# Kernel optimization log

Hardware: AMD Instinct MI355X
Metric: run time of the kernel (lower is better)

## Reference

```python
import jax, jax.numpy as jnp
import numpy as np

B, S, D, H = 64, 256, 2048, 16
HD = D // H

def setup_inputs() -> dict:
    key = jax.random.key(0)
    k1, k2, k3 = jax.random.split(key, 3)
    x = jax.random.normal(k1, (B, S, D), dtype=jnp.float32)
    # torch Linear weights: [out_features, in_features], scaled like kaiming-ish init
    w_qkv = jax.random.normal(k2, (3 * D, D), dtype=jnp.float32) * (1.0 / np.sqrt(D))
    w_o = jax.random.normal(k3, (D, D), dtype=jnp.float32) * (1.0 / np.sqrt(D))
    return {"x": x, "w_qkv": w_qkv, "w_o": w_o}

def reference(x, w_qkv, w_o):
    b, s, d = x.shape
    qkv = jnp.einsum('bsd,ed->bse', x, w_qkv)            # [B,S,3D]
    qkv = qkv.reshape(b, s, 3, H, HD).transpose(2, 0, 3, 1, 4)  # [3,B,H,S,HD]
    q, k, v = qkv[0], qkv[1], qkv[2]
    scores = jnp.einsum('bhqd,bhkd->bhqk', q, k) * (HD ** -0.5)  # [B,H,S,S]
    causal = jnp.triu(jnp.ones((s, s), dtype=bool), 1)
    scores = jnp.where(causal, jnp.float32(-1e9), scores)
    a = jax.nn.softmax(scores, axis=-1)
    ctx = jnp.einsum('bhqk,bhkd->bhqd', a, v)            # [B,H,S,HD]
    ctx = ctx.transpose(0, 2, 1, 3).reshape(b, s, d)     # [B,S,D]
    return jnp.einsum('bsd,ed->bse', ctx, w_o)
```

## Files before the change

### kernel.cpp

```cpp
#include <hip/hip_runtime.h>

#define NB 64
#define NS 256
#define ND 2048
#define NH 16
#define NHD 128

typedef unsigned short ushort_t;
typedef __attribute__((ext_vector_type(8))) __bf16 bf16x8;
typedef __attribute__((ext_vector_type(4))) short shortx4;
typedef __attribute__((ext_vector_type(4))) float f32x4;
typedef __attribute__((ext_vector_type(4))) unsigned short ushortx4;

__device__ __forceinline__ unsigned short f2bf(float f) {
  union { float f; unsigned int u; } v; v.f = f;
  unsigned int r = v.u + 0x7FFFu + ((v.u >> 16) & 1u);
  return (unsigned short)(r >> 16);
}

__device__ __forceinline__ void gload16(const void* g, void* l) {
  __builtin_amdgcn_global_load_lds(
      (__attribute__((address_space(1))) void*)(void*)(g),
      (__attribute__((address_space(3))) void*)(l), 16, 0, 0);
}

__global__ void cast_f32_bf16(const float* __restrict__ in, ushort_t* __restrict__ out, long n) {
  long i = ((long)blockIdx.x * blockDim.x + threadIdx.x) * 4;
  if (i + 3 < n) {
    float4 v = *reinterpret_cast<const float4*>(in + i);
    ushortx4 o;
    o.x = f2bf(v.x); o.y = f2bf(v.y); o.z = f2bf(v.z); o.w = f2bf(v.w);
    *reinterpret_cast<ushortx4*>(out + i) = o;
  }
}

template<int MODE>
__global__ __launch_bounds__(512, 2) void gemm256(const ushort_t* __restrict__ A,
                                                  const ushort_t* __restrict__ Bt,
                                                  float* __restrict__ Cf,
                                                  ushort_t* __restrict__ Cq,
                                                  int M, int N, int K) {
  extern __shared__ char smem[];
  const int tid = threadIdx.x;
  const int wv = tid >> 6, lane = tid & 63;
  const int l15 = lane & 15, lg = lane >> 4;
  const int wm = wv >> 2, wn = wv & 3;

  const int nbn = N >> 8;
  const int nwg = (M >> 8) * nbn;
  const int bid = blockIdx.x;
  const int q8 = nwg >> 3, r8 = nwg & 7;
  const int xcd = bid & 7, lin = bid >> 3;
  const int wg = (xcd < r8 ? xcd * (q8 + 1) : r8 * (q8 + 1) + (xcd - r8) * q8) + lin;
  const int m0 = (wg / nbn) << 8;
  const int n0 = (wg % nbn) << 8;

  const int srow = tid >> 3;
  const int sce = ((tid & 7) * 8) ^ ((srow & 7) << 3);
  const ushort_t* pa = A  + (long)(m0 + srow) * K + sce;
  const ushort_t* pb = Bt + (long)(n0 + srow) * K + sce;

  const int cx = (l15 & 7) << 4;
  const int c0 = (lg * 16) ^ cx;
  const int c1 = (64 + lg * 16) ^ cx;

  f32x4 acc[8][4] = {};
  const int nkt = K >> 6;

  #pragma unroll
  for (int ch = 0; ch < 4; ++ch) {
    gload16(pa + (long)(ch * 64) * K, smem + ch * 8192 + wv * 1024);
    gload16(pb + (long)(ch * 64) * K, smem + 32768 + ch * 8192 + wv * 1024);
  }
  asm volatile("s_waitcnt vmcnt(0)" ::: "memory");
  __builtin_amdgcn_s_barrier();

  for (int t = 0; t < nkt; ++t) {
    const char* rb = smem + (t & 1) * 65536;
    if (t + 1 < nkt) {
      char* db = smem + ((t + 1) & 1) * 65536 + wv * 1024;
      const long ko = (long)(t + 1) * 64;
      #pragma unroll
      for (int ch = 0; ch < 4; ++ch) {
        gload16(pa + (long)(ch * 64) * K + ko, db + ch * 8192);
        gload16(pb + (long)(ch * 64) * K + ko, db + 32768 + ch * 8192);
      }
    }
    bf16x8 af[8][2], bf[4][2];
    #pragma unroll
    for (int i = 0; i < 8; ++i) {
      const char* base = rb + (wm * 128 + i * 16 + l15) * 128;
      af[i][0] = *reinterpret_cast<const bf16x8*>(base + c0);
      af[i][1] = *reinterpret_cast<const bf16x8*>(base + c1);
    }
    #pragma unroll
    for (int j = 0; j < 4; ++j) {
      const char* base = rb + 32768 + (wn * 64 + j * 16 + l15) * 128;
      bf[j][0] = *reinterpret_cast<const bf16x8*>(base + c0);
      bf[j][1] = *reinterpret_cast<const bf16x8*>(base + c1);
    }
    asm volatile("s_waitcnt lgkmcnt(0)" ::: "memory");
    __builtin_amdgcn_sched_barrier(0);
    __builtin_amdgcn_s_setprio(1);
    #pragma unroll
    for (int kk = 0; kk < 2; ++kk)
      #pragma unroll
      for (int i = 0; i < 8; ++i)
        #pragma unroll
        for (int j = 0; j < 4; ++j)
          acc[i][j] = __builtin_amdgcn_mfma_f32_16x16x32_bf16(af[i][kk], bf[j][kk], acc[i][j], 0, 0, 0);
    __builtin_amdgcn_s_setprio(0);
    __builtin_amdgcn_sched_barrier(0);
    asm volatile("s_waitcnt vmcnt(0)" ::: "memory");
    __builtin_amdgcn_s_barrier();
  }

  #pragma unroll
  for (int k = 0; k < 8; ++k) {
    const int mrow = m0 + wm * 128 + k * 16 + lg * 4;
    #pragma unroll
    for (int j = 0; j < 4; ++j) {
      const int n = n0 + wn * 64 + j * 16 + l15;
      #pragma unroll
      for (int r = 0; r < 4; ++r) {
        const int m = mrow + r;
        const float v = acc[k][j][r];
        if (MODE == 0) {
          Cf[(long)m * N + n] = v;
        } else {
          const int tq = n >> 11, hh = (n >> 7) & 15, hd = n & 127;
          const int b = m >> 8, s = m & 255;
          Cq[((((long)tq * NB + b) * NH + hh) * NS + s) * NHD + hd] = f2bf(v);
        }
      }
    }
  }
}

__global__ __launch_bounds__(512) void attn_fused(const ushort_t* __restrict__ qkv,
                                                  ushort_t* __restrict__ ctx) {
  const int bh = blockIdx.x;
  const int b = bh >> 4, h = bh & 15;
  const int wave = threadIdx.x >> 6, lane = threadIdx.x & 63;
  const int l15 = lane & 15, lg = lane >> 4;
  const long head_off = ((long)(b * NH + h)) * (NS * NHD);
  const ushort_t* Qp = qkv + head_off;
  const ushort_t* Kp = qkv + (long)NB * NH * NS * NHD + head_off;
  const ushort_t* Vp = qkv + 2L * NB * NH * NS * NHD + head_off;
  const int q0 = wave * 32;

  bf16x8 qf[2][4];
  #pragma unroll
  for (int ni = 0; ni < 2; ++ni)
    #pragma unroll
    for (int kk = 0; kk < 4; ++kk)
      qf[ni][kk] = *reinterpret_cast<const bf16x8*>(Qp + (q0 + ni * 16 + l15) * NHD + kk * 32 + lg * 8);

  f32x4 o[8][2] = {};
  float mstate[2] = {-1e30f, -1e30f};
  float lstate[2] = {0.f, 0.f};
  const float scale = 0.08838834764831845f;
  const int ntiles = (q0 + 32 + 63) >> 6;

  for (int kt = 0; kt < ntiles; ++kt) {
    f32x4 st[4][2] = {};
    #pragma unroll
    for (int kk = 0; kk < 4; ++kk) {
      bf16x8 kf[4];
      #pragma unroll
      for (int mi = 0; mi < 4; ++mi)
        kf[mi] = *reinterpret_cast<const bf16x8*>(Kp + (kt * 64 + mi * 16 + l15) * NHD + kk * 32 + lg * 8);
      #pragma unroll
      for (int mi = 0; mi < 4; ++mi)
        #pragma unroll
        for (int ni = 0; ni < 2; ++ni)
          st[mi][ni] = __builtin_amdgcn_mfma_f32_16x16x32_bf16(kf[mi], qf[ni][kk], st[mi][ni], 0, 0, 0);
    }
    const bool last = (kt == ntiles - 1);
    #pragma unroll
    for (int mi = 0; mi < 4; ++mi)
      #pragma unroll
      for (int ni = 0; ni < 2; ++ni)
        #pragma unroll
        for (int r = 0; r < 4; ++r) {
          const int kc = kt * 64 + mi * 16 + lg * 4 + r;
          const int q = q0 + ni * 16 + l15;
          float v = st[mi][ni][r] * scale;
          if (last && kc > q) v = -1e30f;
          st[mi][ni][r] = v;
        }
    shortx4 p[4][2];
    #pragma unroll
    for (int ni = 0; ni < 2; ++ni) {
      float tmax = -1e30f;
      #pragma unroll
      for (int mi = 0; mi < 4; ++mi)
        #pragma unroll
        for (int r = 0; r < 4; ++r) tmax = fmaxf(tmax, st[mi][ni][r]);
      tmax = fmaxf(tmax, __shfl_xor(tmax, 16, 64));
      tmax = fmaxf(tmax, __shfl_xor(tmax, 32, 64));
      const float mnew = fmaxf(mstate[ni], tmax);
      const float alpha = __expf(mstate[ni] - mnew);
      float tsum = 0.f;
      #pragma unroll
      for (int mi = 0; mi < 4; ++mi)
        #pragma unroll
        for (int r = 0; r < 4; ++r) {
          const float pe = __expf(st[mi][ni][r] - mnew);
          st[mi][ni][r] = pe;
          tsum += pe;
        }
      tsum += __shfl_xor(tsum, 16, 64);
      tsum += __shfl_xor(tsum, 32, 64);
      lstate[ni] = lstate[ni] * alpha + tsum;
      mstate[ni] = mnew;
      #pragma unroll
      for (int f = 0; f < 8; ++f)
        #pragma unroll
        for (int r = 0; r < 4; ++r) o[f][ni][r] *= alpha;
      #pragma unroll
      for (int mi = 0; mi < 4; ++mi)
        #pragma unroll
        for (int r = 0; r < 4; ++r) p[mi][ni][r] = (short)f2bf(st[mi][ni][r]);
    }
    #pragma unroll
    for (int f = 0; f < 8; ++f)
      #pragma unroll
      for (int mi = 0; mi < 4; ++mi) {
        shortx4 vt;
        #pragma unroll
        for (int j = 0; j < 4; ++j)
          vt[j] = (short)Vp[(kt * 64 + mi * 16 + lg * 4 + j) * NHD + f * 16 + l15];
        #pragma unroll
        for (int ni = 0; ni < 2; ++ni)
          o[f][ni] = __builtin_amdgcn_mfma_f32_16x16x16bf16_1k(vt, p[mi][ni], o[f][ni], 0, 0, 0);
      }
  }
  const float inv0 = 1.f / lstate[0], inv1 = 1.f / lstate[1];
  #pragma unroll
  for (int f = 0; f < 8; ++f)
    #pragma unroll
    for (int ni = 0; ni < 2; ++ni) {
      const float inv = ni ? inv1 : inv0;
      const int q = q0 + ni * 16 + l15;
      const int hd = f * 16 + lg * 4;
      ushortx4 ov;
      #pragma unroll
      for (int r = 0; r < 4; ++r) ov[r] = f2bf(o[f][ni][r] * inv);
      *reinterpret_cast<ushortx4*>(ctx + ((long)(b * NS + q)) * ND + h * NHD + hd) = ov;
    }
}

extern "C" void kernel_launch(void* const* d_in, const int* in_sizes, int n_in,
                              void* d_out, int out_size, void* d_ws, size_t ws_size,
                              hipStream_t stream) {
  const float* x     = (const float*)d_in[0];
  const float* w_qkv = (const float*)d_in[1];
  const float* w_o   = (const float*)d_in[2];
  char* ws = (char*)d_ws;
  if (ws_size < 369098752UL) return;
  ushort_t* xb    = (ushort_t*)(ws);
  ushort_t* wqkvb = (ushort_t*)(ws + 67108864L);
  ushort_t* wob   = (ushort_t*)(ws + 92274688L);
  ushort_t* qkvb  = (ushort_t*)(ws + 100663296L);
  ushort_t* ctxb  = (ushort_t*)(ws + 301989888L);

  const long nx = (long)NB * NS * ND;
  const long nq = 3L * ND * ND;
  const long no = (long)ND * ND;
  cast_f32_bf16<<<dim3(nx / 1024), 256, 0, stream>>>(x, xb, nx);
  cast_f32_bf16<<<dim3(nq / 1024), 256, 0, stream>>>(w_qkv, wqkvb, nq);
  cast_f32_bf16<<<dim3(no / 1024), 256, 0, stream>>>(w_o, wob, no);

  const int lds_bytes = 2 * 65536;
  (void)hipFuncSetAttribute(reinterpret_cast<const void*>(&gemm256<1>),
                            hipFuncAttributeMaxDynamicSharedMemorySize, lds_bytes);
  (void)hipFuncSetAttribute(reinterpret_cast<const void*>(&gemm256<0>),
                            hipFuncAttributeMaxDynamicSharedMemorySize, lds_bytes);

  gemm256<1><<<dim3(64 * 24), 512, lds_bytes, stream>>>(xb, wqkvb, nullptr, qkvb,
                                                        NB * NS, 3 * ND, ND);
  attn_fused<<<dim3(NB * NH), 512, 0, stream>>>(qkvb, ctxb);
  gemm256<0><<<dim3(64 * 8), 512, lds_bytes, stream>>>(ctxb, wob, (float*)d_out, nullptr,
                                                       NB * NS, ND, ND);
}
```

Before: 673.5 us.

## Load GEMM B operand directly from global into registers, halve LDS

The GEMM kernel no longer stages the B (weight) tile through LDS. Each wave loads its B fragments straight from global memory into registers, while only the A tile stays double-buffered in LDS, which halves LDS use to 64KB. The k-step is split into two MFMA halves with partial waitcnts, so the second half's LDS reads overlap the first half's MFMAs. The cost is that each B element is now fetched from global or L2 once per wave that needs it, not once per block, and the global load latency now sits right before the MFMAs.

```diff
diff --git a/kernel.cpp b/kernel.cpp
--- a/kernel.cpp
+++ b/kernel.cpp
@@ -57,58 +57,67 @@
 
   const int srow = tid >> 3;
   const int sce = ((tid & 7) * 8) ^ ((srow & 7) << 3);
-  const ushort_t* pa = A  + (long)(m0 + srow) * K + sce;
-  const ushort_t* pb = Bt + (long)(n0 + srow) * K + sce;
+  const ushort_t* pa = A + (long)(m0 + srow) * K + sce;
 
   const int cx = (l15 & 7) << 4;
   const int c0 = (lg * 16) ^ cx;
   const int c1 = (64 + lg * 16) ^ cx;
 
+  const ushort_t* pbase = Bt + (long)(n0 + wn * 64 + l15) * K + lg * 8;
+
   f32x4 acc[8][4] = {};
   const int nkt = K >> 6;
 
   #pragma unroll
-  for (int ch = 0; ch < 4; ++ch) {
+  for (int ch = 0; ch < 4; ++ch)
     gload16(pa + (long)(ch * 64) * K, smem + ch * 8192 + wv * 1024);
-    gload16(pb + (long)(ch * 64) * K, smem + 32768 + ch * 8192 + wv * 1024);
-  }
   asm volatile("s_waitcnt vmcnt(0)" ::: "memory");
   __builtin_amdgcn_s_barrier();
 
   for (int t = 0; t < nkt; ++t) {
-    const char* rb = smem + (t & 1) * 65536;
+    const char* rb = smem + (t & 1) * 32768;
+    const long kof = (long)t * 64;
+    bf16x8 b0[4], b1[4];
+    #pragma unroll
+    for (int j = 0; j < 4; ++j)
+      b0[j] = *reinterpret_cast<const bf16x8*>(pbase + (long)(j * 16) * K + kof);
+    #pragma unroll
+    for (int j = 0; j < 4; ++j)
+      b1[j] = *reinterpret_cast<const bf16x8*>(pbase + (long)(j * 16) * K + kof + 32);
+    __builtin_amdgcn_sched_barrier(0);
     if (t + 1 < nkt) {
-      char* db = smem + ((t + 1) & 1) * 65536 + wv * 1024;
-      const long ko = (long)(t + 1) * 64;
-      #pragma unroll
-      for (int ch = 0; ch < 4; ++ch) {
-        gload16(pa + (long)(ch * 64) * K + ko, db + ch * 8192);
-        gload16(pb + (long)(ch * 64) * K + ko, db + 32768 + ch * 8192);
-      }
-    }
-    bf16x8 af[8][2], bf[4][2];
-    #pragma unroll
-    for (int i = 0; i < 8; ++i) {
-      const char* base = rb + (wm * 128 + i * 16 + l15) * 128;
-      af[i][0] = *reinterpret_cast<const bf16x8*>(base + c0);
-      af[i][1] = *reinterpret_cast<const bf16x8*>(base + c1);
-    }
-    #pragma unroll
-    for (int j = 0; j < 4; ++j) {
-      const char* base = rb + 32768 + (wn * 64 + j * 16 + l15) * 128;
-      bf[j][0] = *reinterpret_cast<const bf16x8*>(base + c0);
-      bf[j][1] = *reinterpret_cast<const bf16x8*>(base + c1);
-    }
+      char* db = smem + ((t + 1) & 1) * 32768 + wv * 1024;
+      #pragma unroll
+      for (int ch = 0; ch < 4; ++ch)
+        gload16(pa + (long)(ch * 64) * K + kof + 64, db + ch * 8192);
+    }
+    __builtin_amdgcn_sched_barrier(0);
+    bf16x8 a0[8], a1[8];
+    #pragma unroll
+    for (int i = 0; i < 8; ++i)
+      a0[i] = *reinterpret_cast<const bf16x8*>(rb + (wm * 128 + i * 16 + l15) * 128 + c0);
+    #pragma unroll
+    for (int i = 0; i < 8; ++i)
+      a1[i] = *reinterpret_cast<const bf16x8*>(rb + (wm * 128 + i * 16 + l15) * 128 + c1);
+    if (t + 1 < nkt)
+      asm volatile("s_waitcnt vmcnt(4) lgkmcnt(8)" ::: "memory");
+    else
+      asm volatile("s_waitcnt vmcnt(0) lgkmcnt(8)" ::: "memory");
+    __builtin_amdgcn_sched_barrier(0);
+    __builtin_amdgcn_s_setprio(1);
+    #pragma unroll
+    for (int i = 0; i < 8; ++i)
+      #pragma unroll
+      for (int j = 0; j < 4; ++j)
+        acc[i][j] = __builtin_amdgcn_mfma_f32_16x16x32_bf16(a0[i], b0[j], acc[i][j], 0, 0, 0);
+    __builtin_amdgcn_sched_barrier(0);
     asm volatile("s_waitcnt lgkmcnt(0)" ::: "memory");
     __builtin_amdgcn_sched_barrier(0);
-    __builtin_amdgcn_s_setprio(1);
-    #pragma unroll
-    for (int kk = 0; kk < 2; ++kk)
-      #pragma unroll
-      for (int i = 0; i < 8; ++i)
-        #pragma unroll
-        for (int j = 0; j < 4; ++j)
-          acc[i][j] = __builtin_amdgcn_mfma_f32_16x16x32_bf16(af[i][kk], bf[j][kk], acc[i][j], 0, 0, 0);
+    #pragma unroll
+    for (int i = 0; i < 8; ++i)
+      #pragma unroll
+      for (int j = 0; j < 4; ++j)
+        acc[i][j] = __builtin_amdgcn_mfma_f32_16x16x32_bf16(a1[i], b1[j], acc[i][j], 0, 0, 0);
     __builtin_amdgcn_s_setprio(0);
     __builtin_amdgcn_sched_barrier(0);
     asm volatile("s_waitcnt vmcnt(0)" ::: "memory");
@@ -272,7 +281,7 @@
   cast_f32_bf16<<<dim3(nq / 1024), 256, 0, stream>>>(w_qkv, wqkvb, nq);
   cast_f32_bf16<<<dim3(no / 1024), 256, 0, stream>>>(w_o, wob, no);
 
-  const int lds_bytes = 2 * 65536;
+  const int lds_bytes = 2 * 32768;
   (void)hipFuncSetAttribute(reinterpret_cast<const void*>(&gemm256<1>),
                             hipFuncAttributeMaxDynamicSharedMemorySize, lds_bytes);
   (void)hipFuncSetAttribute(reinterpret_cast<const void*>(&gemm256<0>),
```

Result: slower. 1.001 ms (+48.6%).

## Split GEMM k-step into four interleaved phases of LDS reads, prefetch, and MFMA

Applied to the files above, without the earlier changes.

The inner GEMM loop is restructured so that each k-tile is processed in four quadrant phases. Each phase issues a subset of the LDS fragment reads and global-to-LDS prefetches, then runs a block of MFMAs, with barriers between phases. The aim is to overlap memory traffic with matrix compute and cut fragment register pressure (a[4][2], b[4][2] instead of af[8][2], bf[4][2]). In exchange there are several extra block barriers per iteration, which could add synchronization stalls.

```diff
diff --git a/kernel.cpp b/kernel.cpp
--- a/kernel.cpp
+++ b/kernel.cpp
@@ -77,38 +77,102 @@
 
   for (int t = 0; t < nkt; ++t) {
     const char* rb = smem + (t & 1) * 65536;
-    if (t + 1 < nkt) {
-      char* db = smem + ((t + 1) & 1) * 65536 + wv * 1024;
-      const long ko = (long)(t + 1) * 64;
-      #pragma unroll
-      for (int ch = 0; ch < 4; ++ch) {
-        gload16(pa + (long)(ch * 64) * K + ko, db + ch * 8192);
-        gload16(pb + (long)(ch * 64) * K + ko, db + 32768 + ch * 8192);
-      }
-    }
-    bf16x8 af[8][2], bf[4][2];
-    #pragma unroll
-    for (int i = 0; i < 8; ++i) {
-      const char* base = rb + (wm * 128 + i * 16 + l15) * 128;
-      af[i][0] = *reinterpret_cast<const bf16x8*>(base + c0);
-      af[i][1] = *reinterpret_cast<const bf16x8*>(base + c1);
-    }
-    #pragma unroll
-    for (int j = 0; j < 4; ++j) {
-      const char* base = rb + 32768 + (wn * 64 + j * 16 + l15) * 128;
-      bf[j][0] = *reinterpret_cast<const bf16x8*>(base + c0);
-      bf[j][1] = *reinterpret_cast<const bf16x8*>(base + c1);
-    }
+    char* db = smem + ((t + 1) & 1) * 65536 + wv * 1024;
+    const long ko = (long)(t + 1) * 64;
+    const bool pf = (t + 1 < nkt);
+    bf16x8 a[4][2], b[4][2];
+    const char* abase = rb + (wm * 128 + l15) * 128;
+    const char* bbase = rb + 32768 + (wn * 64 + l15) * 128;
+
+    #pragma unroll
+    for (int i = 0; i < 4; ++i) {
+      a[i][0] = *reinterpret_cast<const bf16x8*>(abase + i * 16 * 128 + c0);
+      a[i][1] = *reinterpret_cast<const bf16x8*>(abase + i * 16 * 128 + c1);
+    }
+    #pragma unroll
+    for (int j = 0; j < 2; ++j) {
+      b[j][0] = *reinterpret_cast<const bf16x8*>(bbase + j * 16 * 128 + c0);
+      b[j][1] = *reinterpret_cast<const bf16x8*>(bbase + j * 16 * 128 + c1);
+    }
+    if (pf) {
+      gload16(pa + ko, db);
+      gload16(pa + (long)64 * K + ko, db + 8192);
+    }
+    asm volatile("s_waitcnt lgkmcnt(8)" ::: "memory");
+    __builtin_amdgcn_s_barrier();
     asm volatile("s_waitcnt lgkmcnt(0)" ::: "memory");
     __builtin_amdgcn_sched_barrier(0);
     __builtin_amdgcn_s_setprio(1);
     #pragma unroll
     for (int kk = 0; kk < 2; ++kk)
       #pragma unroll
-      for (int i = 0; i < 8; ++i)
-        #pragma unroll
-        for (int j = 0; j < 4; ++j)
-          acc[i][j] = __builtin_amdgcn_mfma_f32_16x16x32_bf16(af[i][kk], bf[j][kk], acc[i][j], 0, 0, 0);
+      for (int i = 0; i < 4; ++i)
+        #pragma unroll
+        for (int j = 0; j < 2; ++j)
+          acc[i][j] = __builtin_amdgcn_mfma_f32_16x16x32_bf16(a[i][kk], b[j][kk], acc[i][j], 0, 0, 0);
+    __builtin_amdgcn_s_setprio(0);
+    __builtin_amdgcn_s_barrier();
+
+    #pragma unroll
+    for (int j = 2; j < 4; ++j) {
+      b[j][0] = *reinterpret_cast<const bf16x8*>(bbase + j * 16 * 128 + c0);
+      b[j][1] = *reinterpret_cast<const bf16x8*>(bbase + j * 16 * 128 + c1);
+    }
+    if (pf) {
+      gload16(pa + (long)128 * K + ko, db + 16384);
+      gload16(pa + (long)192 * K + ko, db + 24576);
+    }
+    __builtin_amdgcn_s_barrier();
+    asm volatile("s_waitcnt lgkmcnt(0)" ::: "memory");
+    __builtin_amdgcn_sched_barrier(0);
+    __builtin_amdgcn_s_setprio(1);
+    #pragma unroll
+    for (int kk = 0; kk < 2; ++kk)
+      #pragma unroll
+      for (int i = 0; i < 4; ++i)
+        #pragma unroll
+        for (int j = 2; j < 4; ++j)
+          acc[i][j] = __builtin_amdgcn_mfma_f32_16x16x32_bf16(a[i][kk], b[j][kk], acc[i][j], 0, 0, 0);
+    __builtin_amdgcn_s_setprio(0);
+    __builtin_amdgcn_s_barrier();
+
+    #pragma unroll
+    for (int i = 0; i < 4; ++i) {
+      a[i][0] = *reinterpret_cast<const bf16x8*>(abase + (64 + i * 16) * 128 + c0);
+      a[i][1] = *reinterpret_cast<const bf16x8*>(abase + (64 + i * 16) * 128 + c1);
+    }
+    if (pf) {
+      gload16(pb + ko, db + 32768);
+      gload16(pb + (long)64 * K + ko, db + 32768 + 8192);
+    }
+    __builtin_amdgcn_s_barrier();
+    asm volatile("s_waitcnt lgkmcnt(0)" ::: "memory");
+    __builtin_amdgcn_sched_barrier(0);
+    __builtin_amdgcn_s_setprio(1);
+    #pragma unroll
+    for (int kk = 0; kk < 2; ++kk)
+      #pragma unroll
+      for (int i = 0; i < 4; ++i)
+        #pragma unroll
+        for (int j = 0; j < 2; ++j)
+          acc[4 + i][j] = __builtin_amdgcn_mfma_f32_16x16x32_bf16(a[i][kk], b[j][kk], acc[4 + i][j], 0, 0, 0);
+    __builtin_amdgcn_s_setprio(0);
+    __builtin_amdgcn_s_barrier();
+
+    if (pf) {
+      gload16(pb + (long)128 * K + ko, db + 32768 + 16384);
+      gload16(pb + (long)192 * K + ko, db + 32768 + 24576);
+    }
+    __builtin_amdgcn_s_barrier();
+    __builtin_amdgcn_sched_barrier(0);
+    __builtin_amdgcn_s_setprio(1);
+    #pragma unroll
+    for (int kk = 0; kk < 2; ++kk)
+      #pragma unroll
+      for (int i = 0; i < 4; ++i)
+        #pragma unroll
+        for (int j = 2; j < 4; ++j)
+          acc[4 + i][j] = __builtin_amdgcn_mfma_f32_16x16x32_bf16(a[i][kk], b[j][kk], acc[4 + i][j], 0, 0, 0);
     __builtin_amdgcn_s_setprio(0);
     __builtin_amdgcn_sched_barrier(0);
     asm volatile("s_waitcnt vmcnt(0)" ::: "memory");
```

New measurement: 698.5 us. 1.04x slower.

## Stage V tiles in LDS with transpose reads; fuse cast kernels

Applied to the files above, without the earlier changes.

The attention kernel now double-buffers the V tile in shared memory using async global-to-LDS loads. It then reads V with ds_read_b64_tr_b16 transpose loads for the PV MFMAs, replacing the old per-element strided scalar global gathers. Every wave now runs all four key tiles so block barriers stay uniform, and waves past their causal limit skip the compute. The three f32-to-bf16 cast launches are merged into one, and the GEMM prefetch offset is rewritten. The cost is extra barriers and idle iterations for early waves, and occupancy is bounded at 2 blocks.

```diff
diff --git a/kernel.cpp b/kernel.cpp
--- a/kernel.cpp
+++ b/kernel.cpp
@@ -24,14 +24,31 @@
       (__attribute__((address_space(3))) void*)(l), 16, 0, 0);
 }
 
-__global__ void cast_f32_bf16(const float* __restrict__ in, ushort_t* __restrict__ out, long n) {
-  long i = ((long)blockIdx.x * blockDim.x + threadIdx.x) * 4;
-  if (i + 3 < n) {
-    float4 v = *reinterpret_cast<const float4*>(in + i);
-    ushortx4 o;
-    o.x = f2bf(v.x); o.y = f2bf(v.y); o.z = f2bf(v.z); o.w = f2bf(v.w);
-    *reinterpret_cast<ushortx4*>(out + i) = o;
-  }
+__device__ __forceinline__ unsigned lds_off(const void* p) {
+  return (unsigned)(size_t)(__attribute__((address_space(3))) const void*)p;
+}
+
+template<int OFF>
+__device__ __forceinline__ shortx4 tr16(unsigned addr) {
+  shortx4 d;
+  asm volatile("ds_read_b64_tr_b16 %0, %1 offset:%2"
+               : "=v"(d) : "v"(addr), "i"(OFF));
+  return d;
+}
+
+__global__ void cast3_f32_bf16(const float* __restrict__ x, const float* __restrict__ wq,
+                               const float* __restrict__ wo, ushort_t* __restrict__ xb,
+                               ushort_t* __restrict__ wqb, ushort_t* __restrict__ wob) {
+  long bi = blockIdx.x;
+  const float* src; ushort_t* dst;
+  if (bi < 32768) { src = x; dst = xb; }
+  else if (bi < 32768 + 12288) { bi -= 32768; src = wq; dst = wqb; }
+  else { bi -= 32768 + 12288; src = wo; dst = wob; }
+  const long i = (bi * 256 + threadIdx.x) * 4;
+  float4 v = *reinterpret_cast<const float4*>(src + i);
+  ushortx4 o;
+  o.x = f2bf(v.x); o.y = f2bf(v.y); o.z = f2bf(v.z); o.w = f2bf(v.w);
+  *reinterpret_cast<ushortx4*>(dst + i) = o;
 }
 
 template<int MODE>
@@ -77,13 +94,13 @@
 
   for (int t = 0; t < nkt; ++t) {
     const char* rb = smem + (t & 1) * 65536;
+    const long kof = (long)t * 64;
     if (t + 1 < nkt) {
       char* db = smem + ((t + 1) & 1) * 65536 + wv * 1024;
-      const long ko = (long)(t + 1) * 64;
       #pragma unroll
       for (int ch = 0; ch < 4; ++ch) {
-        gload16(pa + (long)(ch * 64) * K + ko, db + ch * 8192);
-        gload16(pb + (long)(ch * 64) * K + ko, db + 32768 + ch * 8192);
+        gload16(pa + (long)(ch * 64) * K + kof + 64, db + ch * 8192);
+        gload16(pb + (long)(ch * 64) * K + kof + 64, db + 32768 + ch * 8192);
       }
     }
     bf16x8 af[8][2], bf[4][2];
@@ -137,17 +154,25 @@
   }
 }
 
-__global__ __launch_bounds__(512) void attn_fused(const ushort_t* __restrict__ qkv,
-                                                  ushort_t* __restrict__ ctx) {
+__global__ __launch_bounds__(512, 2) void attn_fused(const ushort_t* __restrict__ qkv,
+                                                     ushort_t* __restrict__ ctx) {
+  __shared__ char vsm[32768];
   const int bh = blockIdx.x;
   const int b = bh >> 4, h = bh & 15;
-  const int wave = threadIdx.x >> 6, lane = threadIdx.x & 63;
+  const int tid = threadIdx.x;
+  const int wave = tid >> 6, lane = tid & 63;
   const int l15 = lane & 15, lg = lane >> 4;
   const long head_off = ((long)(b * NH + h)) * (NS * NHD);
   const ushort_t* Qp = qkv + head_off;
   const ushort_t* Kp = qkv + (long)NB * NH * NS * NHD + head_off;
   const ushort_t* Vp = qkv + 2L * NB * NH * NS * NHD + head_off;
   const int q0 = wave * 32;
+  const int klast = (q0 + 31) >> 6;
+
+  const int t7 = tid & 127;
+  const int srowv = ((t7 >> 3) << 2) | ((t7 >> 1) & 3);
+  const int vcol = (tid >> 7) * 16 + (t7 & 1) * 8;
+  const ushort_t* vsrc = Vp + srowv * NHD + vcol;
 
   bf16x8 qf[2][4];
   #pragma unroll
@@ -160,82 +185,106 @@
   float mstate[2] = {-1e30f, -1e30f};
   float lstate[2] = {0.f, 0.f};
   const float scale = 0.08838834764831845f;
-  const int ntiles = (q0 + 32 + 63) >> 6;
-
-  for (int kt = 0; kt < ntiles; ++kt) {
-    f32x4 st[4][2] = {};
-    #pragma unroll
-    for (int kk = 0; kk < 4; ++kk) {
-      bf16x8 kf[4];
+
+  gload16(vsrc, vsm + wave * 1024);
+  gload16(vsrc + 64, vsm + 8192 + wave * 1024);
+  asm volatile("s_waitcnt vmcnt(0)" ::: "memory");
+  __builtin_amdgcn_s_barrier();
+
+  for (int kt = 0; kt < 4; ++kt) {
+    if (kt + 1 < 4) {
+      char* db = vsm + ((kt + 1) & 1) * 16384 + wave * 1024;
+      const ushort_t* s = vsrc + (kt + 1) * 64 * NHD;
+      gload16(s, db);
+      gload16(s + 64, db + 8192);
+    }
+    shortx4 p[4][2];
+    const bool act = (kt <= klast);
+    if (act) {
+      f32x4 st[4][2] = {};
+      #pragma unroll
+      for (int kk = 0; kk < 4; ++kk) {
+        bf16x8 kf[4];
+        #pragma unroll
+        for (int mi = 0; mi < 4; ++mi)
+          kf[mi] = *reinterpret_cast<const bf16x8*>(Kp + (kt * 64 + mi * 16 + l15) * NHD + kk * 32 + lg * 8);
+        #pragma unroll
+        for (int mi = 0; mi < 4; ++mi)
+          #pragma unroll
+          for (int ni = 0; ni < 2; ++ni)
+            st[mi][ni] = __builtin_amdgcn_mfma_f32_16x16x32_bf16(kf[mi], qf[ni][kk], st[mi][ni], 0, 0, 0);
+      }
+      const bool dom = (kt == klast);
       #pragma unroll
       for (int mi = 0; mi < 4; ++mi)
-        kf[mi] = *reinterpret_cast<const bf16x8*>(Kp + (kt * 64 + mi * 16 + l15) * NHD + kk * 32 + lg * 8);
-      #pragma unroll
-      for (int mi = 0; mi < 4; ++mi)
         #pragma unroll
         for (int ni = 0; ni < 2; ++ni)
-          st[mi][ni] = __builtin_amdgcn_mfma_f32_16x16x32_bf16(kf[mi], qf[ni][kk], st[mi][ni], 0, 0, 0);
-    }
-    const bool last = (kt == ntiles - 1);
-    #pragma unroll
-    for (int mi = 0; mi < 4; ++mi)
-      #pragma unroll
-      for (int ni = 0; ni < 2; ++ni)
-        #pragma unroll
-        for (int r = 0; r < 4; ++r) {
-          const int kc = kt * 64 + mi * 16 + lg * 4 + r;
-          const int q = q0 + ni * 16 + l15;
-          float v = st[mi][ni][r] * scale;
-          if (last && kc > q) v = -1e30f;
-          st[mi][ni][r] = v;
-        }
-    shortx4 p[4][2];
-    #pragma unroll
-    for (int ni = 0; ni < 2; ++ni) {
-      float tmax = -1e30f;
-      #pragma unroll
-      for (int mi = 0; mi < 4; ++mi)
-        #pragma unroll
-        for (int r = 0; r < 4; ++r) tmax = fmaxf(tmax, st[mi][ni][r]);
-      tmax = fmaxf(tmax, __shfl_xor(tmax, 16, 64));
-      tmax = fmaxf(tmax, __shfl_xor(tmax, 32, 64));
-      const float mnew = fmaxf(mstate[ni], tmax);
-      const float alpha = __expf(mstate[ni] - mnew);
-      float tsum = 0.f;
-      #pragma unroll
-      for (int mi = 0; mi < 4; ++mi)
-        #pragma unroll
-        for (int r = 0; r < 4; ++r) {
-          const float pe = __expf(st[mi][ni][r] - mnew);
-          st[mi][ni][r] = pe;
-          tsum += pe;
-        }
-      tsum += __shfl_xor(tsum, 16, 64);
-      tsum += __shfl_xor(tsum, 32, 64);
-      lstate[ni] = lstate[ni] * alpha + tsum;
-      mstate[ni] = mnew;
-      #pragma unroll
-      for (int f = 0; f < 8; ++f)
-        #pragma unroll
-        for (int r = 0; r < 4; ++r) o[f][ni][r] *= alpha;
-      #pragma unroll
-      for (int mi = 0; mi < 4; ++mi)
-        #pragma unroll
-        for (int r = 0; r < 4; ++r) p[mi][ni][r] = (short)f2bf(st[mi][ni][r]);
-    }
-    #pragma unroll
-    for (int f = 0; f < 8; ++f)
-      #pragma unroll
-      for (int mi = 0; mi < 4; ++mi) {
-        shortx4 vt;
-        #pragma unroll
-        for (int j = 0; j < 4; ++j)
-          vt[j] = (short)Vp[(kt * 64 + mi * 16 + lg * 4 + j) * NHD + f * 16 + l15];
-        #pragma unroll
-        for (int ni = 0; ni < 2; ++ni)
-          o[f][ni] = __builtin_amdgcn_mfma_f32_16x16x16bf16_1k(vt, p[mi][ni], o[f][ni], 0, 0, 0);
-      }
+          #pragma unroll
+          for (int r = 0; r < 4; ++r) {
+            const int kc = kt * 64 + mi * 16 + lg * 4 + r;
+            const int q = q0 + ni * 16 + l15;
+            float v = st[mi][ni][r] * scale;
+            if (dom && kc > q) v = -1e30f;
+            st[mi][ni][r] = v;
+          }
+      #pragma unroll
+      for (int ni = 0; ni < 2; ++ni) {
+        float tmax = -1e30f;
+        #pragma unroll
+        for (int mi = 0; mi < 4; ++mi)
+          #pragma unroll
+          for (int r = 0; r < 4; ++r) tmax = fmaxf(tmax, st[mi][ni][r]);
+        tmax = fmaxf(tmax, __shfl_xor(tmax, 16, 64));
+        tmax = fmaxf(tmax, __shfl_xor(tmax, 32, 64));
+        const float mnew = fmaxf(mstate[ni], tmax);
+        const float alpha = __expf(mstate[ni] - mnew);
+        float tsum = 0.f;
+        #pragma unroll
+        for (int mi = 0; mi < 4; ++mi)
+          #pragma unroll
+          for (int r = 0; r < 4; ++r) {
+            const float pe = __expf(st[mi][ni][r] - mnew);
+            st[mi][ni][r] = pe;
+            tsum += pe;
+          }
+        tsum += __shfl_xor(tsum, 16, 64);
+        tsum += __shfl_xor(tsum, 32, 64);
+        lstate[ni] = lstate[ni] * alpha + tsum;
+        mstate[ni] = mnew;
+        #pragma unroll
+        for (int f = 0; f < 8; ++f)
+          #pragma unroll
+          for (int r = 0; r < 4; ++r) o[f][ni][r] *= alpha;
+        #pragma unroll
+        for (int mi = 0; mi < 4; ++mi)
+          #pragma unroll
+          for (int r = 0; r < 4; ++r) p[mi][ni][r] = (short)f2bf(st[mi][ni][r]);
+      }
+      const unsigned va = lds_off(vsm) + (unsigned)((kt & 1) * 16384 + lane * 8);
+#define PVF(F)                                                                  \
+      {                                                                         \
+        shortx4 v0 = tr16<(F)*2048 +    0>(va);                                 \
+        shortx4 v1 = tr16<(F)*2048 +  512>(va);                                 \
+        shortx4 v2 = tr16<(F)*2048 + 1024>(va);                                 \
+        shortx4 v3 = tr16<(F)*2048 + 1536>(va);                                 \
+        asm volatile("s_waitcnt lgkmcnt(0)" ::: "memory");                      \
+        __builtin_amdgcn_sched_barrier(0);                                      \
+        o[F][0] = __builtin_amdgcn_mfma_f32_16x16x16bf16_1k(v0, p[0][0], o[F][0], 0, 0, 0); \
+        o[F][1] = __builtin_amdgcn_mfma_f32_16x16x16bf16_1k(v0, p[0][1], o[F][1], 0, 0, 0); \
+        o[F][0] = __builtin_amdgcn_mfma_f32_16x16x16bf16_1k(v1, p[1][0], o[F][0], 0, 0, 0); \
+        o[F][1] = __builtin_amdgcn_mfma_f32_16x16x16bf16_1k(v1, p[1][1], o[F][1], 0, 0, 0); \
+        o[F][0] = __builtin_amdgcn_mfma_f32_16x16x16bf16_1k(v2, p[2][0], o[F][0], 0, 0, 0); \
+        o[F][1] = __builtin_amdgcn_mfma_f32_16x16x16bf16_1k(v2, p[2][1], o[F][1], 0, 0, 0); \
+        o[F][0] = __builtin_amdgcn_mfma_f32_16x16x16bf16_1k(v3, p[3][0], o[F][0], 0, 0, 0); \
+        o[F][1] = __builtin_amdgcn_mfma_f32_16x16x16bf16_1k(v3, p[3][1], o[F][1], 0, 0, 0); \
+      }
+      PVF(0) PVF(1) PVF(2) PVF(3) PVF(4) PVF(5) PVF(6) PVF(7)
+#undef PVF
+    }
+    asm volatile("s_waitcnt vmcnt(0)" ::: "memory");
+    __builtin_amdgcn_s_barrier();
   }
+
   const float inv0 = 1.f / lstate[0], inv1 = 1.f / lstate[1];
   #pragma unroll
   for (int f = 0; f < 8; ++f)
@@ -265,12 +314,7 @@
   ushort_t* qkvb  = (ushort_t*)(ws + 100663296L);
   ushort_t* ctxb  = (ushort_t*)(ws + 301989888L);
 
-  const long nx = (long)NB * NS * ND;
-  const long nq = 3L * ND * ND;
-  const long no = (long)ND * ND;
-  cast_f32_bf16<<<dim3(nx / 1024), 256, 0, stream>>>(x, xb, nx);
-  cast_f32_bf16<<<dim3(nq / 1024), 256, 0, stream>>>(w_qkv, wqkvb, nq);
-  cast_f32_bf16<<<dim3(no / 1024), 256, 0, stream>>>(w_o, wob, no);
+  cast3_f32_bf16<<<dim3(49152), 256, 0, stream>>>(x, w_qkv, w_o, xb, wqkvb, wob);
 
   const int lds_bytes = 2 * 65536;
   (void)hipFuncSetAttribute(reinterpret_cast<const void*>(&gemm256<1>),
```

Result: no change. 674.7 us (+0.2%).
